# Optimization experiments

Measured on AMD Instinct MI355X. Metric: run time of the kernel, lower is better.

The kernel has to match this reference:

```python
import jax, jax.numpy as jnp
import numpy as np

N, E = 50000, 800000
IN_DIM, HID = 11, 128
EPS = 1e-5

def setup_inputs() -> dict:
    key = jax.random.key(0)
    ks = jax.random.split(key, 20)
    def w(k, i, o):
        return jax.random.normal(k, (i, o), jnp.float32) * (1.0 / np.sqrt(i))
    inp = {}
    inp['x'] = jax.random.normal(ks[0], (N, IN_DIM), jnp.float32)
    inp['edge_index'] = jax.random.randint(ks[1], (2, E), 0, N, jnp.int64)
    dims = [(IN_DIM, HID), (HID, HID), (HID, HID)]
    for i, (di, do) in enumerate(dims):
        inp[f'w_l{i}'] = w(ks[2 + 3 * i], di, do)
        inp[f'b_l{i}'] = jnp.zeros((do,), jnp.float32)
        inp[f'w_r{i}'] = w(ks[3 + 3 * i], di, do)
        inp[f'ln_w{i}'] = jnp.ones((do,), jnp.float32)
        inp[f'ln_b{i}'] = jnp.zeros((do,), jnp.float32)
    inp['c_w0'] = w(ks[12], HID, HID // 2)
    inp['c_b0'] = jnp.zeros((HID // 2,), jnp.float32)
    inp['c_w1'] = w(ks[13], HID // 2, 1)
    inp['c_b1'] = jnp.zeros((1,), jnp.float32)
    return inp

def _sage_conv(x, src, dst, w_l, b_l, w_r):
    # PyG SAGEConv (mean aggr): lin_l(mean_{j in N(i)} x_j) + lin_r(x_i)
    n = x.shape[0]
    agg = jax.ops.segment_sum(x[src], dst, num_segments=n)
    cnt = jax.ops.segment_sum(jnp.ones((src.shape[0], 1), x.dtype), dst, num_segments=n)
    agg = agg / jnp.maximum(cnt, 1.0)
    return agg @ w_l + b_l + x @ w_r

def _layernorm(h, w, b):
    mu = jnp.mean(h, axis=-1, keepdims=True)
    var = jnp.mean(jnp.square(h - mu), axis=-1, keepdims=True)
    return (h - mu) * jax.lax.rsqrt(var + EPS) * w + b

def reference(x, edge_index, w_l0, b_l0, w_r0, ln_w0, ln_b0,
              w_l1, b_l1, w_r1, ln_w1, ln_b1,
              w_l2, b_l2, w_r2, ln_w2, ln_b2,
              c_w0, c_b0, c_w1, c_b1):
    src, dst = edge_index[0], edge_index[1]
    layers = [(w_l0, b_l0, w_r0, ln_w0, ln_b0),
              (w_l1, b_l1, w_r1, ln_w1, ln_b1),
              (w_l2, b_l2, w_r2, ln_w2, ln_b2)]
    for i, (wl, bl, wr, gw, gb) in enumerate(layers):
        h = _sage_conv(x, src, dst, wl, bl, wr)
        h = jax.nn.relu(_layernorm(h, gw, gb))
        # dropout is identity in eval mode
        if i > 0 and h.shape == x.shape:
            h = h + x
        x = h
    h = jax.nn.relu(x @ c_w0 + c_b0)
    out = h @ c_w1 + c_b1
    return out.squeeze(-1)
```

## Files before the change

kernel.cpp:

```cpp
#include <hip/hip_runtime.h>
#include <hip/hip_fp16.h>

#define HID 128

typedef _Float16 h2_t __attribute__((ext_vector_type(2)));
typedef _Float16 half8 __attribute__((ext_vector_type(8)));
typedef float f32x4 __attribute__((ext_vector_type(4)));

static __device__ __forceinline__ float fdot2(__half2 a, __half2 b, float c) {
    return __builtin_amdgcn_fdot2(__builtin_bit_cast(h2_t, a), __builtin_bit_cast(h2_t, b), c, false);
}

__global__ __launch_bounds__(256) void zero_kernel(int4* __restrict__ p, int n4) {
    int i = blockIdx.x * 256 + threadIdx.x;
    if (i < n4) p[i] = make_int4(0, 0, 0, 0);
}

__global__ __launch_bounds__(256) void deg_kernel(const int* __restrict__ ei,
                                                  int* __restrict__ deg, int E, int n) {
    int grp  = blockIdx.x & 7;
    int blk  = blockIdx.x >> 3;
    int nblk = gridDim.x >> 3;
    int lo = (int)(((long long)n * grp) >> 3);
    int hi = (int)(((long long)n * (grp + 1)) >> 3);
    for (int e = blk * 256 + threadIdx.x; e < E; e += nblk * 256) {
        int dst = ei[E + e];
        if (dst >= lo && dst < hi) atomicAdd(&deg[dst], 1);
    }
}

__global__ __launch_bounds__(256) void part_kernel(const int* __restrict__ deg,
                                                   int* __restrict__ part, int n) {
    int i = blockIdx.x * 256 + threadIdx.x;
    int v = (i < n) ? deg[i] : 0;
    #pragma unroll
    for (int m = 1; m < 64; m <<= 1) v += __shfl_xor(v, m);
    __shared__ int w[4];
    int lane = threadIdx.x & 63, wv = threadIdx.x >> 6;
    if (lane == 0) w[wv] = v;
    __syncthreads();
    if (threadIdx.x == 0) part[blockIdx.x] = w[0] + w[1] + w[2] + w[3];
}

__global__ __launch_bounds__(1024) void scanpart_kernel(int* __restrict__ part, int nb) {
    __shared__ int s[1024];
    int t = threadIdx.x;
    int v = (t < nb) ? part[t] : 0;
    int orig = v;
    s[t] = v;
    __syncthreads();
    for (int off = 1; off < 1024; off <<= 1) {
        int u = (t >= off) ? s[t - off] : 0;
        __syncthreads();
        s[t] += u;
        __syncthreads();
    }
    if (t < nb) part[t] = s[t] - orig;
}

__global__ __launch_bounds__(256) void rp_kernel(const int* __restrict__ deg,
                                                 const int* __restrict__ part,
                                                 int* __restrict__ rp,
                                                 int* __restrict__ cursor, int n) {
    int tid = threadIdx.x, lane = tid & 63, wv = tid >> 6;
    int i = blockIdx.x * 256 + tid;
    int v = (i < n) ? deg[i] : 0;
    int orig = v;
    #pragma unroll
    for (int off = 1; off < 64; off <<= 1) {
        int t = __shfl_up(v, off);
        if (lane >= off) v += t;
    }
    __shared__ int wsum[4];
    if (lane == 63) wsum[wv] = v;
    __syncthreads();
    int wbase = 0;
    #pragma unroll
    for (int w = 0; w < 4; ++w) if (w < wv) wbase += wsum[w];
    int excl = part[blockIdx.x] + wbase + v - orig;
    if (i < n) { rp[i] = excl; cursor[i] = excl; }
    if (i == n - 1) rp[n] = excl + orig;
}

__global__ __launch_bounds__(256) void fill_kernel(const int* __restrict__ ei,
                                                   int* __restrict__ cursor,
                                                   int* __restrict__ csr_src, int E, int n) {
    int grp  = blockIdx.x & 7;
    int blk  = blockIdx.x >> 3;
    int nblk = gridDim.x >> 3;
    int lo = (int)(((long long)n * grp) >> 3);
    int hi = (int)(((long long)n * (grp + 1)) >> 3);
    for (int e = blk * 256 + threadIdx.x; e < E; e += nblk * 256) {
        int dst = ei[E + e];
        if (dst >= lo && dst < hi) {
            int pos = atomicAdd(&cursor[dst], 1);
            csr_src[pos] = ei[e];
        }
    }
}

__global__ __launch_bounds__(256) void aggp_kernel(const int* __restrict__ rp,
                                                   const int* __restrict__ ci,
                                                   const __half* __restrict__ h16,
                                                   __half* __restrict__ agg16, int n) {
    int node = (blockIdx.x * 256 + threadIdx.x) >> 6;
    if (node >= n) return;
    int lane = threadIdx.x & 63;
    float2 a0 = make_float2(0.f, 0.f), a1 = make_float2(0.f, 0.f);
    float2 a2 = make_float2(0.f, 0.f), a3 = make_float2(0.f, 0.f);
    float2 a4 = make_float2(0.f, 0.f), a5 = make_float2(0.f, 0.f);
    float2 a6 = make_float2(0.f, 0.f), a7 = make_float2(0.f, 0.f);
    int beg = rp[node], end = rp[node + 1];
    int j = beg;
    for (; j + 7 < end; j += 8) {
        int s0 = ci[j],     s1 = ci[j + 1], s2 = ci[j + 2], s3 = ci[j + 3];
        int s4 = ci[j + 4], s5 = ci[j + 5], s6 = ci[j + 6], s7 = ci[j + 7];
        float2 f0 = __half22float2(*(const __half2*)(h16 + (size_t)s0 * HID + lane * 2));
        float2 f1 = __half22float2(*(const __half2*)(h16 + (size_t)s1 * HID + lane * 2));
        float2 f2 = __half22float2(*(const __half2*)(h16 + (size_t)s2 * HID + lane * 2));
        float2 f3 = __half22float2(*(const __half2*)(h16 + (size_t)s3 * HID + lane * 2));
        float2 f4 = __half22float2(*(const __half2*)(h16 + (size_t)s4 * HID + lane * 2));
        float2 f5 = __half22float2(*(const __half2*)(h16 + (size_t)s5 * HID + lane * 2));
        float2 f6 = __half22float2(*(const __half2*)(h16 + (size_t)s6 * HID + lane * 2));
        float2 f7 = __half22float2(*(const __half2*)(h16 + (size_t)s7 * HID + lane * 2));
        a0.x += f0.x; a0.y += f0.y;  a1.x += f1.x; a1.y += f1.y;
        a2.x += f2.x; a2.y += f2.y;  a3.x += f3.x; a3.y += f3.y;
        a4.x += f4.x; a4.y += f4.y;  a5.x += f5.x; a5.y += f5.y;
        a6.x += f6.x; a6.y += f6.y;  a7.x += f7.x; a7.y += f7.y;
    }
    for (; j + 3 < end; j += 4) {
        int s0 = ci[j], s1 = ci[j + 1], s2 = ci[j + 2], s3 = ci[j + 3];
        float2 f0 = __half22float2(*(const __half2*)(h16 + (size_t)s0 * HID + lane * 2));
        float2 f1 = __half22float2(*(const __half2*)(h16 + (size_t)s1 * HID + lane * 2));
        float2 f2 = __half22float2(*(const __half2*)(h16 + (size_t)s2 * HID + lane * 2));
        float2 f3 = __half22float2(*(const __half2*)(h16 + (size_t)s3 * HID + lane * 2));
        a0.x += f0.x; a0.y += f0.y;  a1.x += f1.x; a1.y += f1.y;
        a2.x += f2.x; a2.y += f2.y;  a3.x += f3.x; a3.y += f3.y;
    }
    for (; j < end; ++j) {
        int s0 = ci[j];
        float2 f0 = __half22float2(*(const __half2*)(h16 + (size_t)s0 * HID + lane * 2));
        a0.x += f0.x; a0.y += f0.y;
    }
    float inv = 1.0f / fmaxf((float)(end - beg), 1.0f);
    float ox = (a0.x + a1.x + a2.x + a3.x + a4.x + a5.x + a6.x + a7.x) * inv;
    float oy = (a0.y + a1.y + a2.y + a3.y + a4.y + a5.y + a6.y + a7.y) * inv;
    *(__half2*)(agg16 + (size_t)node * HID + lane * 2) = __floats2half2_rn(ox, oy);
}

__global__ __launch_bounds__(256) void layer0_kernel(
    const float* __restrict__ x, const int* __restrict__ rp, const int* __restrict__ ci,
    const float* __restrict__ w_l, const float* __restrict__ b_l, const float* __restrict__ w_r,
    const float* __restrict__ ln_w, const float* __restrict__ ln_b,
    __half* __restrict__ h16, int n)
{
    int node = (blockIdx.x * 256 + threadIdx.x) >> 6;
    int lane = threadIdx.x & 63;
    if (node >= n) return;
    int beg = rp[node], end = rp[node + 1];
    int g = lane / 11;
    int d = lane - g * 11;
    float acc0 = 0.f, acc1 = 0.f;
    int j = beg + g;
    if (g < 5) {
        for (; j + 5 < end; j += 10) {
            int s0 = ci[j], s1 = ci[j + 5];
            acc0 += x[(size_t)s0 * 11 + d];
            acc1 += x[(size_t)s1 * 11 + d];
        }
        for (; j < end; j += 5) {
            int s0 = ci[j];
            acc0 += x[(size_t)s0 * 11 + d];
        }
    }
    float acc = acc0 + acc1;
    float aggk = 0.f;
    #pragma unroll
    for (int gg = 0; gg < 5; ++gg) {
        aggk += __shfl(acc, (lane < 11) ? (lane + 11 * gg) : lane);
    }
    float inv = 1.0f / fmaxf((float)(end - beg), 1.0f);
    float v0 = b_l[lane], v1 = b_l[lane + 64];
    #pragma unroll
    for (int k = 0; k < 11; ++k) {
        float a  = __shfl(aggk, k) * inv;
        float xi = x[(size_t)node * 11 + k];
        v0 += a * w_l[k * HID + lane]      + xi * w_r[k * HID + lane];
        v1 += a * w_l[k * HID + lane + 64] + xi * w_r[k * HID + lane + 64];
    }
    float s = v0 + v1, s2 = v0 * v0 + v1 * v1;
    #pragma unroll
    for (int m = 1; m < 64; m <<= 1) { s += __shfl_xor(s, m); s2 += __shfl_xor(s2, m); }
    float mu  = s * (1.0f / HID);
    float var = s2 * (1.0f / HID) - mu * mu;
    float rstd = rsqrtf(var + 1e-5f);
    float o0 = fmaxf((v0 - mu) * rstd * ln_w[lane]      + ln_b[lane],      0.0f);
    float o1 = fmaxf((v1 - mu) * rstd * ln_w[lane + 64] + ln_b[lane + 64], 0.0f);
    h16[(size_t)node * HID + lane]      = __float2half_rn(o0);
    h16[(size_t)node * HID + lane + 64] = __float2half_rn(o1);
}

__global__ __launch_bounds__(256) void wfrag_kernel(const float* __restrict__ wl,
                                                    const float* __restrict__ wr,
                                                    __half* __restrict__ wf) {
    int idx = blockIdx.x * 256 + threadIdx.x;
    if (idx >= 4096) return;
    int kt = idx >> 9;
    int ct = (idx >> 6) & 7;
    int l  = idx & 63;
    int col = ct * 16 + (l & 15);
    int kbase = kt * 32 + (l >> 4) * 8;
    #pragma unroll
    for (int j = 0; j < 8; ++j) {
        int k = kbase + j;
        const float* W = (k < HID) ? wl : wr;
        int kk = k & (HID - 1);
        wf[(size_t)idx * 8 + j] = __float2half_rn(W[kk * HID + col]);
    }
}

__global__ __launch_bounds__(256) void wpack_cls_kernel(const float* __restrict__ w0,
                                                        __half2* __restrict__ w0p) {
    int idx = blockIdx.x * 256 + threadIdx.x;
    if (idx >= 64 * 64) return;
    int p = idx >> 6, c = idx & 63;
    w0p[idx] = __floats2half2_rn(w0[(2 * p) * 64 + c], w0[(2 * p + 1) * 64 + c]);
}

__global__ __launch_bounds__(256) void layer_kernel(
    const __half* __restrict__ agg16, const __half* __restrict__ h16in,
    const __half* __restrict__ wf, const float* __restrict__ b_l,
    const float* __restrict__ ln_w, const float* __restrict__ ln_b,
    __half* __restrict__ h16out, int n)
{
    __shared__ __half lds[64][264];
    int base = blockIdx.x * 64;
    int tid = threadIdx.x;
    #pragma unroll
    for (int i = 0; i < 8; ++i) {
        int idx = tid + i * 256;
        int row = idx >> 5;
        int c4  = (idx & 31) * 4;
        int node = base + row;
        float2 a = make_float2(0.f, 0.f);
        float2 h = make_float2(0.f, 0.f);
        if (node < n) {
            a = *(const float2*)(agg16 + (size_t)node * HID + c4);
            h = *(const float2*)(h16in + (size_t)node * HID + c4);
        }
        *(float2*)&lds[row][c4]       = a;
        *(float2*)&lds[row][HID + c4] = h;
    }
    __syncthreads();

    int w = tid >> 6;
    int l = tid & 63;
    int g = l >> 4, cl = l & 15;

    f32x4 acc[8];
    #pragma unroll
    for (int ct = 0; ct < 8; ++ct) acc[ct] = (f32x4){0.f, 0.f, 0.f, 0.f};

    #pragma unroll
    for (int kt = 0; kt < 8; ++kt) {
        half8 a = *(const half8*)&lds[w * 16 + cl][kt * 32 + g * 8];
        #pragma unroll
        for (int ct = 0; ct < 8; ++ct) {
            half8 b = *(const half8*)(wf + ((size_t)(kt * 8 + ct) * 64 + l) * 8);
            acc[ct] = __builtin_amdgcn_mfma_f32_16x16x32_f16(a, b, acc[ct], 0, 0, 0);
        }
    }

    float bl8[8], gw8[8], gb8[8];
    #pragma unroll
    for (int ct = 0; ct < 8; ++ct) {
        bl8[ct] = b_l[ct * 16 + cl];
        gw8[ct] = ln_w[ct * 16 + cl];
        gb8[ct] = ln_b[ct * 16 + cl];
    }

    #pragma unroll
    for (int r = 0; r < 4; ++r) {
        int row = w * 16 + g * 4 + r;
        float v[8];
        float s = 0.f, s2 = 0.f;
        #pragma unroll
        for (int ct = 0; ct < 8; ++ct) {
            v[ct] = acc[ct][r] + bl8[ct];
            s += v[ct]; s2 += v[ct] * v[ct];
        }
        #pragma unroll
        for (int m = 1; m < 16; m <<= 1) { s += __shfl_xor(s, m); s2 += __shfl_xor(s2, m); }
        float mu  = s * (1.0f / HID);
        float var = s2 * (1.0f / HID) - mu * mu;
        float rstd = rsqrtf(var + 1e-5f);
        int node = base + row;
        if (node < n) {
            #pragma unroll
            for (int ct = 0; ct < 8; ++ct) {
                float o = fmaxf((v[ct] - mu) * rstd * gw8[ct] + gb8[ct], 0.f)
                          + __half2float(lds[row][HID + ct * 16 + cl]);
                h16out[(size_t)node * HID + ct * 16 + cl] = __float2half_rn(o);
            }
        }
    }
}

__global__ __launch_bounds__(256) void cls_kernel(
    const __half* __restrict__ h, const __half2* __restrict__ w0p, const float* __restrict__ b0,
    const float* __restrict__ w1, const float* __restrict__ b1, float* __restrict__ out, int n)
{
    __shared__ __half2 w0s[64 * 64];
    int tid = threadIdx.x;
    #pragma unroll
    for (int i = 0; i < 16; ++i) w0s[tid + i * 256] = w0p[tid + i * 256];
    __syncthreads();
    int lane = tid & 63, wv = tid >> 6;
    float bb0 = b0[lane], ww1 = w1[lane], bb1 = b1[0];
    #pragma unroll 1
    for (int q = 0; q < 4; ++q) {
        int node = blockIdx.x * 16 + wv * 4 + q;
        if (node >= n) break;
        const __half2* hr = (const __half2*)(h + (size_t)node * HID);
        float s0 = 0.f, s1 = 0.f;
        #pragma unroll
        for (int p = 0; p < 64; p += 2) {
            s0 = fdot2(hr[p],     w0s[(p + 0) * 64 + lane], s0);
            s1 = fdot2(hr[p + 1], w0s[(p + 1) * 64 + lane], s1);
        }
        float s = fmaxf(s0 + s1 + bb0, 0.f);
        float t = s * ww1;
        #pragma unroll
        for (int m = 1; m < 64; m <<= 1) t += __shfl_xor(t, m);
        if (lane == 0) out[node] = t + bb1;
    }
}

extern "C" void kernel_launch(void* const* d_in, const int* in_sizes, int n_in,
                              void* d_out, int out_size, void* d_ws, size_t ws_size,
                              hipStream_t stream) {
    const float* x  = (const float*)d_in[0];
    const int*   ei = (const int*)d_in[1];
    const float* w_l0 = (const float*)d_in[2];
    const float* b_l0 = (const float*)d_in[3];
    const float* w_r0 = (const float*)d_in[4];
    const float* lnw0 = (const float*)d_in[5];
    const float* lnb0 = (const float*)d_in[6];
    const float* w_l1 = (const float*)d_in[7];
    const float* b_l1 = (const float*)d_in[8];
    const float* w_r1 = (const float*)d_in[9];
    const float* lnw1 = (const float*)d_in[10];
    const float* lnb1 = (const float*)d_in[11];
    const float* w_l2 = (const float*)d_in[12];
    const float* b_l2 = (const float*)d_in[13];
    const float* w_r2 = (const float*)d_in[14];
    const float* lnw2 = (const float*)d_in[15];
    const float* lnb2 = (const float*)d_in[16];
    const float* c_w0 = (const float*)d_in[17];
    const float* c_b0 = (const float*)d_in[18];
    const float* c_w1 = (const float*)d_in[19];
    const float* c_b1 = (const float*)d_in[20];
    float* out = (float*)d_out;

    int N = in_sizes[0] / 11;
    int E = in_sizes[1] / 2;
    int nb = (N + 255) / 256;

    int*     deg    = (int*)d_ws;
    int*     rp     = deg + N;
    int*     cursor = rp + (N + 1);
    int*     csr    = cursor + N;
    int*     part   = csr + E;
    __half*  h16    = (__half*)(part + ((nb + 63) & ~63));
    __half*  agg16  = h16 + (size_t)N * HID;
    __half*  wf1    = agg16 + (size_t)N * HID;
    __half*  wf2    = wf1 + 4096 * 8;
    __half2* w0p    = (__half2*)(wf2 + 4096 * 8);

    int n4 = (N + 3) / 4;
    zero_kernel<<<(n4 + 255) / 256, 256, 0, stream>>>((int4*)deg, n4);
    deg_kernel<<<8 * 512, 256, 0, stream>>>(ei, deg, E, N);
    part_kernel<<<nb, 256, 0, stream>>>(deg, part, N);
    scanpart_kernel<<<1, 1024, 0, stream>>>(part, nb);
    rp_kernel<<<nb, 256, 0, stream>>>(deg, part, rp, cursor, N);
    fill_kernel<<<8 * 512, 256, 0, stream>>>(ei, cursor, csr, E, N);
    wfrag_kernel<<<16, 256, 0, stream>>>(w_l1, w_r1, wf1);
    wfrag_kernel<<<16, 256, 0, stream>>>(w_l2, w_r2, wf2);
    wpack_cls_kernel<<<16, 256, 0, stream>>>(c_w0, w0p);

    int nodeBlocks = (N + 3) / 4;

    layer0_kernel<<<nodeBlocks, 256, 0, stream>>>(x, rp, csr, w_l0, b_l0, w_r0, lnw0, lnb0, h16, N);

    aggp_kernel<<<nodeBlocks, 256, 0, stream>>>(rp, csr, h16, agg16, N);
    layer_kernel<<<(N + 63) / 64, 256, 0, stream>>>(agg16, h16, wf1, b_l1, lnw1, lnb1, h16, N);

    aggp_kernel<<<nodeBlocks, 256, 0, stream>>>(rp, csr, h16, agg16, N);
    layer_kernel<<<(N + 63) / 64, 256, 0, stream>>>(agg16, h16, wf2, b_l2, lnw2, lnb2, h16, N);

    cls_kernel<<<(N + 15) / 16, 256, 0, stream>>>(h16, w0p, c_b0, c_w1, c_b1, out, N);
}
```

Measured before the change: 269.1 us.

## Vectorize neighbor gathers, restructure layer0 aggregation, and give cls blocks more nodes

The aggregation kernel now splits each wavefront into two halves that process alternate edges, with each lane loading 4 halves (8 bytes) per neighbor row; the halves are combined with a cross-lane shuffle before the store. Layer0 aggregation now has each lane take whole edges and sum all 11 input features, followed by 11 full-wave butterfly reductions, replacing the 5-group per-feature scheme. The classifier kernel processes 8 nodes per wave instead of 4, halving the grid and amortizing the shared-memory weight load. Risks include extra shuffle cost in layer0 and less load balance for low-degree nodes.

```diff
diff --git a/kernel.cpp b/kernel.cpp
--- a/kernel.cpp
+++ b/kernel.cpp
@@ -106,46 +106,57 @@
     int node = (blockIdx.x * 256 + threadIdx.x) >> 6;
     if (node >= n) return;
     int lane = threadIdx.x & 63;
-    float2 a0 = make_float2(0.f, 0.f), a1 = make_float2(0.f, 0.f);
-    float2 a2 = make_float2(0.f, 0.f), a3 = make_float2(0.f, 0.f);
-    float2 a4 = make_float2(0.f, 0.f), a5 = make_float2(0.f, 0.f);
-    float2 a6 = make_float2(0.f, 0.f), a7 = make_float2(0.f, 0.f);
+    int half = lane >> 5;
+    int c4 = (lane & 31) * 4;
     int beg = rp[node], end = rp[node + 1];
-    int j = beg;
-    for (; j + 7 < end; j += 8) {
-        int s0 = ci[j],     s1 = ci[j + 1], s2 = ci[j + 2], s3 = ci[j + 3];
-        int s4 = ci[j + 4], s5 = ci[j + 5], s6 = ci[j + 6], s7 = ci[j + 7];
-        float2 f0 = __half22float2(*(const __half2*)(h16 + (size_t)s0 * HID + lane * 2));
-        float2 f1 = __half22float2(*(const __half2*)(h16 + (size_t)s1 * HID + lane * 2));
-        float2 f2 = __half22float2(*(const __half2*)(h16 + (size_t)s2 * HID + lane * 2));
-        float2 f3 = __half22float2(*(const __half2*)(h16 + (size_t)s3 * HID + lane * 2));
-        float2 f4 = __half22float2(*(const __half2*)(h16 + (size_t)s4 * HID + lane * 2));
-        float2 f5 = __half22float2(*(const __half2*)(h16 + (size_t)s5 * HID + lane * 2));
-        float2 f6 = __half22float2(*(const __half2*)(h16 + (size_t)s6 * HID + lane * 2));
-        float2 f7 = __half22float2(*(const __half2*)(h16 + (size_t)s7 * HID + lane * 2));
-        a0.x += f0.x; a0.y += f0.y;  a1.x += f1.x; a1.y += f1.y;
-        a2.x += f2.x; a2.y += f2.y;  a3.x += f3.x; a3.y += f3.y;
-        a4.x += f4.x; a4.y += f4.y;  a5.x += f5.x; a5.y += f5.y;
-        a6.x += f6.x; a6.y += f6.y;  a7.x += f7.x; a7.y += f7.y;
-    }
-    for (; j + 3 < end; j += 4) {
-        int s0 = ci[j], s1 = ci[j + 1], s2 = ci[j + 2], s3 = ci[j + 3];
-        float2 f0 = __half22float2(*(const __half2*)(h16 + (size_t)s0 * HID + lane * 2));
-        float2 f1 = __half22float2(*(const __half2*)(h16 + (size_t)s1 * HID + lane * 2));
-        float2 f2 = __half22float2(*(const __half2*)(h16 + (size_t)s2 * HID + lane * 2));
-        float2 f3 = __half22float2(*(const __half2*)(h16 + (size_t)s3 * HID + lane * 2));
-        a0.x += f0.x; a0.y += f0.y;  a1.x += f1.x; a1.y += f1.y;
-        a2.x += f2.x; a2.y += f2.y;  a3.x += f3.x; a3.y += f3.y;
-    }
-    for (; j < end; ++j) {
+    float4 A0 = make_float4(0.f, 0.f, 0.f, 0.f);
+    float4 A1 = make_float4(0.f, 0.f, 0.f, 0.f);
+    float4 A2 = make_float4(0.f, 0.f, 0.f, 0.f);
+    float4 A3 = make_float4(0.f, 0.f, 0.f, 0.f);
+    int j = beg + half;
+    for (; j + 6 < end; j += 8) {
+        int s0 = ci[j], s1 = ci[j + 2], s2 = ci[j + 4], s3 = ci[j + 6];
+        float2 r0 = *(const float2*)(h16 + (size_t)s0 * HID + c4);
+        float2 r1 = *(const float2*)(h16 + (size_t)s1 * HID + c4);
+        float2 r2 = *(const float2*)(h16 + (size_t)s2 * HID + c4);
+        float2 r3 = *(const float2*)(h16 + (size_t)s3 * HID + c4);
+        const __half2* p0 = (const __half2*)&r0;
+        const __half2* p1 = (const __half2*)&r1;
+        const __half2* p2 = (const __half2*)&r2;
+        const __half2* p3 = (const __half2*)&r3;
+        float2 l0 = __half22float2(p0[0]), h0 = __half22float2(p0[1]);
+        float2 l1 = __half22float2(p1[0]), h1 = __half22float2(p1[1]);
+        float2 l2 = __half22float2(p2[0]), h2 = __half22float2(p2[1]);
+        float2 l3 = __half22float2(p3[0]), h3 = __half22float2(p3[1]);
+        A0.x += l0.x; A0.y += l0.y; A0.z += h0.x; A0.w += h0.y;
+        A1.x += l1.x; A1.y += l1.y; A1.z += h1.x; A1.w += h1.y;
+        A2.x += l2.x; A2.y += l2.y; A2.z += h2.x; A2.w += h2.y;
+        A3.x += l3.x; A3.y += l3.y; A3.z += h3.x; A3.w += h3.y;
+    }
+    for (; j < end; j += 2) {
         int s0 = ci[j];
-        float2 f0 = __half22float2(*(const __half2*)(h16 + (size_t)s0 * HID + lane * 2));
-        a0.x += f0.x; a0.y += f0.y;
-    }
-    float inv = 1.0f / fmaxf((float)(end - beg), 1.0f);
-    float ox = (a0.x + a1.x + a2.x + a3.x + a4.x + a5.x + a6.x + a7.x) * inv;
-    float oy = (a0.y + a1.y + a2.y + a3.y + a4.y + a5.y + a6.y + a7.y) * inv;
-    *(__half2*)(agg16 + (size_t)node * HID + lane * 2) = __floats2half2_rn(ox, oy);
+        float2 r0 = *(const float2*)(h16 + (size_t)s0 * HID + c4);
+        const __half2* p0 = (const __half2*)&r0;
+        float2 l0 = __half22float2(p0[0]), h0 = __half22float2(p0[1]);
+        A0.x += l0.x; A0.y += l0.y; A0.z += h0.x; A0.w += h0.y;
+    }
+    float ax = A0.x + A1.x + A2.x + A3.x;
+    float ay = A0.y + A1.y + A2.y + A3.y;
+    float az = A0.z + A1.z + A2.z + A3.z;
+    float aw = A0.w + A1.w + A2.w + A3.w;
+    ax += __shfl_xor(ax, 32);
+    ay += __shfl_xor(ay, 32);
+    az += __shfl_xor(az, 32);
+    aw += __shfl_xor(aw, 32);
+    if (lane < 32) {
+        float inv = 1.0f / fmaxf((float)(end - beg), 1.0f);
+        __half2 o01 = __floats2half2_rn(ax * inv, ay * inv);
+        __half2 o23 = __floats2half2_rn(az * inv, aw * inv);
+        float2 pack;
+        ((__half2*)&pack)[0] = o01;
+        ((__half2*)&pack)[1] = o23;
+        *(float2*)(agg16 + (size_t)node * HID + c4) = pack;
+    }
 }
 
 __global__ __launch_bounds__(256) void layer0_kernel(
@@ -158,35 +169,30 @@
     int lane = threadIdx.x & 63;
     if (node >= n) return;
     int beg = rp[node], end = rp[node + 1];
-    int g = lane / 11;
-    int d = lane - g * 11;
-    float acc0 = 0.f, acc1 = 0.f;
-    int j = beg + g;
-    if (g < 5) {
-        for (; j + 5 < end; j += 10) {
-            int s0 = ci[j], s1 = ci[j + 5];
-            acc0 += x[(size_t)s0 * 11 + d];
-            acc1 += x[(size_t)s1 * 11 + d];
-        }
-        for (; j < end; j += 5) {
-            int s0 = ci[j];
-            acc0 += x[(size_t)s0 * 11 + d];
-        }
-    }
-    float acc = acc0 + acc1;
-    float aggk = 0.f;
-    #pragma unroll
-    for (int gg = 0; gg < 5; ++gg) {
-        aggk += __shfl(acc, (lane < 11) ? (lane + 11 * gg) : lane);
+    float a[11];
+    #pragma unroll
+    for (int k = 0; k < 11; ++k) a[k] = 0.f;
+    for (int j = beg + lane; j < end; j += 64) {
+        int src = ci[j];
+        const float* xr = x + (size_t)src * 11;
+        #pragma unroll
+        for (int k = 0; k < 11; ++k) a[k] += xr[k];
+    }
+    #pragma unroll
+    for (int k = 0; k < 11; ++k) {
+        float v = a[k];
+        #pragma unroll
+        for (int m = 1; m < 64; m <<= 1) v += __shfl_xor(v, m);
+        a[k] = v;
     }
     float inv = 1.0f / fmaxf((float)(end - beg), 1.0f);
     float v0 = b_l[lane], v1 = b_l[lane + 64];
     #pragma unroll
     for (int k = 0; k < 11; ++k) {
-        float a  = __shfl(aggk, k) * inv;
+        float ak = a[k] * inv;
         float xi = x[(size_t)node * 11 + k];
-        v0 += a * w_l[k * HID + lane]      + xi * w_r[k * HID + lane];
-        v1 += a * w_l[k * HID + lane + 64] + xi * w_r[k * HID + lane + 64];
+        v0 += ak * w_l[k * HID + lane]      + xi * w_r[k * HID + lane];
+        v1 += ak * w_l[k * HID + lane + 64] + xi * w_r[k * HID + lane + 64];
     }
     float s = v0 + v1, s2 = v0 * v0 + v1 * v1;
     #pragma unroll
@@ -318,8 +324,8 @@
     int lane = tid & 63, wv = tid >> 6;
     float bb0 = b0[lane], ww1 = w1[lane], bb1 = b1[0];
     #pragma unroll 1
-    for (int q = 0; q < 4; ++q) {
-        int node = blockIdx.x * 16 + wv * 4 + q;
+    for (int q = 0; q < 8; ++q) {
+        int node = blockIdx.x * 32 + wv * 8 + q;
         if (node >= n) break;
         const __half2* hr = (const __half2*)(h + (size_t)node * HID);
         float s0 = 0.f, s1 = 0.f;
@@ -398,5 +404,5 @@
     aggp_kernel<<<nodeBlocks, 256, 0, stream>>>(rp, csr, h16, agg16, N);
     layer_kernel<<<(N + 63) / 64, 256, 0, stream>>>(agg16, h16, wf2, b_l2, lnw2, lnb2, h16, N);
 
-    cls_kernel<<<(N + 15) / 16, 256, 0, stream>>>(h16, w0p, c_b0, c_w1, c_b1, out, N);
-}
+    cls_kernel<<<(N + 31) / 32, 256, 0, stream>>>(h16, w0p, c_b0, c_w1, c_b1, out, N);
+}
```

After: 280.6 us. 1.04x slower.
